# Kernel tuning notes

Hardware: AMD Instinct MI355X
Metric: run time of the kernel (lower is better)

Reference implementation:

```python
import jax, jax.numpy as jnp
import numpy as np

NEG_BIG = -9e15
ALPHA = 0.2  # LeakyReLU negative slope


def setup_inputs() -> dict:
    key = jax.random.key(0)
    k1, k2, k3, k4 = jax.random.split(key, 4)
    B, N, IN, OUT = 8, 2048, 128, 64
    x = jax.random.normal(k1, (B, N, IN), dtype=jnp.float32)
    adj = jax.random.randint(k2, (B, N, N), 0, 2, dtype=jnp.int32)
    # xavier_uniform with gain=1.414
    lim_W = 1.414 * np.sqrt(6.0 / (IN + OUT))
    W = jax.random.uniform(k3, (IN, OUT), jnp.float32, -lim_W, lim_W)
    lim_a = 1.414 * np.sqrt(6.0 / (2 * OUT + 1))
    a = jax.random.uniform(k4, (2 * OUT, 1), jnp.float32, -lim_a, lim_a)
    return {"x": x, "adj": adj, "W": W, "a": a}


def reference(x, adj, W, a):
    # h: [B, N, out_dim]
    h = jnp.matmul(x, W)
    out_dim = W.shape[1]
    a1 = a[:out_dim, 0]   # applied to h_i (row / destination)
    a2 = a[out_dim:, 0]   # applied to h_j (col / source)
    # e_ij = leakyrelu(h_i . a1 + h_j . a2)  -- avoids the O(B*N*N*2d) concat
    si = jnp.einsum('bnd,d->bn', h, a1)  # [B, N]
    sj = jnp.einsum('bnd,d->bn', h, a2)  # [B, N]
    e = si[:, :, None] + sj[:, None, :]  # [B, N, N]
    e = jnp.where(e > 0, e, ALPHA * e)   # LeakyReLU
    e = jnp.where(adj > 0, e, NEG_BIG)
    attention = jax.nn.softmax(e, axis=-1)  # [B, N, N]
    # dropout p=0.0 (eval mode): identity
    h_prime = jnp.matmul(attention, h)       # [B, N, out_dim]
    return h_prime, attention
```

## Files before the change

kernel.cpp:

```cpp
#include <hip/hip_runtime.h>

#define BB 8
#define NN 2048
#define IND 128
#define OUTD 64
#define ALPHA 0.2f

typedef __attribute__((ext_vector_type(8))) short bf16x8;
typedef __attribute__((ext_vector_type(4))) float f32x4;
typedef unsigned int u32;

__global__ __launch_bounds__(256) void k1_hproj(const float* __restrict__ x,
                                                const float* __restrict__ W,
                                                const float* __restrict__ a,
                                                short* __restrict__ hT_hi,
                                                short* __restrict__ hT_lo,
                                                float* __restrict__ si,
                                                float* __restrict__ sj) {
    __shared__ float Wl[IND * OUTD];
    __shared__ float xl[16][IND];
    __shared__ float tile[16][OUTD + 1];
    int t = threadIdx.x, lane = t & 63, wave = t >> 6;

    const float4* W4 = (const float4*)W;
    float4* Wl4 = (float4*)Wl;
    #pragma unroll
    for (int q = 0; q < 8; ++q) Wl4[t + q * 256] = W4[t + q * 256];

    int row0 = blockIdx.x * 16;
    const float4* x4 = (const float4*)(x + (size_t)row0 * IND);
    float4* xl4 = (float4*)&xl[0][0];
    xl4[t] = x4[t];
    xl4[t + 256] = x4[t + 256];
    __syncthreads();

    float a1v = a[lane];
    float a2v = a[OUTD + lane];

    float acc[4] = {0.f, 0.f, 0.f, 0.f};
    int rbase = wave * 4;
    for (int k = 0; k < IND; k += 4) {
        float4 xv0 = *(const float4*)&xl[rbase + 0][k];
        float4 xv1 = *(const float4*)&xl[rbase + 1][k];
        float4 xv2 = *(const float4*)&xl[rbase + 2][k];
        float4 xv3 = *(const float4*)&xl[rbase + 3][k];
        #pragma unroll
        for (int q = 0; q < 4; ++q) {
            float w = Wl[(k + q) * OUTD + lane];
            acc[0] = fmaf(((const float*)&xv0)[q], w, acc[0]);
            acc[1] = fmaf(((const float*)&xv1)[q], w, acc[1]);
            acc[2] = fmaf(((const float*)&xv2)[q], w, acc[2]);
            acc[3] = fmaf(((const float*)&xv3)[q], w, acc[3]);
        }
    }
    #pragma unroll
    for (int rr = 0; rr < 4; ++rr) {
        size_t grow = (size_t)row0 + rbase + rr;
        tile[rbase + rr][lane] = acc[rr];
        float v1 = acc[rr] * a1v;
        float v2 = acc[rr] * a2v;
        #pragma unroll
        for (int o = 32; o; o >>= 1) {
            v1 += __shfl_xor(v1, o);
            v2 += __shfl_xor(v2, o);
        }
        if (lane == 0) { si[grow] = v1; sj[grow] = v2; }
    }
    __syncthreads();

    int d = t >> 2, kq = (t & 3) * 4;
    int b = row0 >> 11;
    int krow = (row0 & (NN - 1)) + kq;
    float v0 = tile[kq + 0][d], v1 = tile[kq + 1][d];
    float v2 = tile[kq + 2][d], v3 = tile[kq + 3][d];
    u32 b0 = __float_as_uint(v0), b1 = __float_as_uint(v1);
    u32 b2 = __float_as_uint(v2), b3 = __float_as_uint(v3);
    u32 h0 = b0 & 0xffff0000u, h1 = b1 & 0xffff0000u;
    u32 h2 = b2 & 0xffff0000u, h3 = b3 & 0xffff0000u;
    float l0 = v0 - __uint_as_float(h0), l1 = v1 - __uint_as_float(h1);
    float l2 = v2 - __uint_as_float(h2), l3 = v3 - __uint_as_float(h3);
    uint2 hi2, lo2;
    hi2.x = (b0 >> 16) | h1;
    hi2.y = (b2 >> 16) | h3;
    lo2.x = (__float_as_uint(l0) >> 16) | (__float_as_uint(l1) & 0xffff0000u);
    lo2.y = (__float_as_uint(l2) >> 16) | (__float_as_uint(l3) & 0xffff0000u);
    size_t off = ((size_t)b * OUTD + d) * NN + krow;
    *(uint2*)(hT_hi + off) = hi2;
    *(uint2*)(hT_lo + off) = lo2;
}

__global__ __launch_bounds__(256) void k23(const int* __restrict__ adj,
                                           const float* __restrict__ si,
                                           const float* __restrict__ sj,
                                           const short* __restrict__ hT_hi,
                                           const short* __restrict__ hT_lo,
                                           float* __restrict__ attn,
                                           float* __restrict__ hp) {
    __shared__ unsigned char mask_lds[16][264];
    __shared__ float inv_lds[16];
    __shared__ f32x4 red[4][4][64];

    int t = threadIdx.x, lane = t & 63, w = t >> 6;
    int bk = blockIdx.x;
    int b = bk >> 7;
    int i0 = (bk & 127) * 16;
    size_t rowbase = (size_t)b * NN + i0;
    const float* sjb = sj + (size_t)b * NN;

    for (int rr = 0; rr < 4; ++rr) {
        int row = w * 4 + rr;
        size_t grow = rowbase + row;
        float s_i = si[grow];
        const int4* arow = (const int4*)(adj + grow * NN);
        float sum = 0.f;
        #pragma unroll
        for (int pass = 0; pass < 4; ++pass) {
            int jb = pass * 512 + lane * 8;
            int4 a0 = arow[pass * 128 + lane * 2];
            int4 a1 = arow[pass * 128 + lane * 2 + 1];
            float4 s0 = *(const float4*)(sjb + jb);
            float4 s1 = *(const float4*)(sjb + jb + 4);
            int av[8] = {a0.x, a0.y, a0.z, a0.w, a1.x, a1.y, a1.z, a1.w};
            float sv[8] = {s0.x, s0.y, s0.z, s0.w, s1.x, s1.y, s1.z, s1.w};
            unsigned mb = 0;
            #pragma unroll
            for (int q = 0; q < 8; ++q) {
                float e = s_i + sv[q];
                e = e > 0.f ? e : ALPHA * e;
                float pe = __expf(e);
                if (av[q] > 0) { mb |= 1u << q; sum += pe; }
            }
            mask_lds[row][pass * 64 + lane] = (unsigned char)mb;
        }
        #pragma unroll
        for (int o = 32; o; o >>= 1) sum += __shfl_xor(sum, o);
        if (lane == 0) inv_lds[row] = sum > 0.f ? 1.0f / sum : 0.f;
    }
    __syncthreads();

    int m = lane & 15, g = lane >> 4;
    float si_m = si[rowbase + m];
    float inv_m = inv_lds[m];
    float* arow_out = attn + (rowbase + m) * (size_t)NN;
    const short* bh_base = hT_hi + ((size_t)b * OUTD + m) * NN;
    const short* bl_base = hT_lo + ((size_t)b * OUTD + m) * NN;

    f32x4 acc[4];
    #pragma unroll
    for (int tt = 0; tt < 4; ++tt) acc[tt] = (f32x4){0.f, 0.f, 0.f, 0.f};

    for (int step = 0; step < 16; ++step) {
        int jb = w * 512 + step * 32 + g * 8;
        float4 s0 = *(const float4*)(sjb + jb);
        float4 s1 = *(const float4*)(sjb + jb + 4);
        unsigned mb = mask_lds[m][jb >> 3];
        float sv[8] = {s0.x, s0.y, s0.z, s0.w, s1.x, s1.y, s1.z, s1.w};
        float p[8];
        #pragma unroll
        for (int q = 0; q < 8; ++q) {
            float e = si_m + sv[q];
            e = e > 0.f ? e : ALPHA * e;
            float pe = __expf(e) * inv_m;
            p[q] = ((mb >> q) & 1) ? pe : 0.f;
        }
        *(float4*)(arow_out + jb) = make_float4(p[0], p[1], p[2], p[3]);
        *(float4*)(arow_out + jb + 4) = make_float4(p[4], p[5], p[6], p[7]);

        union { bf16x8 v; u32 u[4]; } ph, pl;
        #pragma unroll
        for (int q = 0; q < 4; ++q) {
            u32 c0 = __float_as_uint(p[2 * q]), c1 = __float_as_uint(p[2 * q + 1]);
            u32 t0 = c0 & 0xffff0000u, t1 = c1 & 0xffff0000u;
            float d0 = p[2 * q] - __uint_as_float(t0);
            float d1 = p[2 * q + 1] - __uint_as_float(t1);
            ph.u[q] = (c0 >> 16) | t1;
            pl.u[q] = (__float_as_uint(d0) >> 16) | (__float_as_uint(d1) & 0xffff0000u);
        }

        #pragma unroll
        for (int tt = 0; tt < 4; ++tt) {
            bf16x8 bh = *(const bf16x8*)(bh_base + (size_t)tt * 16 * NN + jb);
            bf16x8 bl = *(const bf16x8*)(bl_base + (size_t)tt * 16 * NN + jb);
            acc[tt] = __builtin_amdgcn_mfma_f32_16x16x32_bf16(ph.v, bh, acc[tt], 0, 0, 0);
            acc[tt] = __builtin_amdgcn_mfma_f32_16x16x32_bf16(ph.v, bl, acc[tt], 0, 0, 0);
            acc[tt] = __builtin_amdgcn_mfma_f32_16x16x32_bf16(pl.v, bh, acc[tt], 0, 0, 0);
        }
    }

    #pragma unroll
    for (int tt = 0; tt < 4; ++tt) red[w][tt][lane] = acc[tt];
    __syncthreads();

    for (int idx = t; idx < 16 * OUTD; idx += 256) {
        int row = idx >> 6, n = idx & 63;
        int ln = (row >> 2) * 16 + (n & 15);
        int reg = row & 3;
        float v = ((const float*)&red[0][n >> 4][ln])[reg]
                + ((const float*)&red[1][n >> 4][ln])[reg]
                + ((const float*)&red[2][n >> 4][ln])[reg]
                + ((const float*)&red[3][n >> 4][ln])[reg];
        hp[(rowbase + row) * OUTD + n] = v;
    }
}

extern "C" void kernel_launch(void* const* d_in, const int* in_sizes, int n_in,
                              void* d_out, int out_size, void* d_ws, size_t ws_size,
                              hipStream_t stream) {
    const float* x   = (const float*)d_in[0];
    const int*   adj = (const int*)d_in[1];
    const float* W   = (const float*)d_in[2];
    const float* a   = (const float*)d_in[3];

    float* out  = (float*)d_out;
    float* hp   = out;
    float* attn = out + (size_t)BB * NN * OUTD;

    char* ws = (char*)d_ws;
    short* hT_hi = (short*)ws;
    short* hT_lo = hT_hi + (size_t)BB * OUTD * NN;
    float* si    = (float*)(hT_lo + (size_t)BB * OUTD * NN);
    float* sj    = si + (size_t)BB * NN;

    k1_hproj<<<BB * NN / 16, 256, 0, stream>>>(x, W, a, hT_hi, hT_lo, si, sj);
    k23<<<BB * NN / 16, 256, 0, stream>>>(adj, si, sj, hT_hi, hT_lo, attn, hp);
}
```

Measured before the change: 130.6 us.

## Split adjacency mask pass into separate kernel and coalesce attention writes

Moves the adjacency scan and softmax denominator computation into its own kernel, which writes a packed bit mask and inverse sums to workspace, using one wave per row across many more blocks. The attention-plus-PV kernel then reads the mask from global memory and writes the attention matrix in a fully coalesced row-major loop rather than the strided per-lane layout tied to the MFMA fragment. The aim is to raise parallelism on the adj-reading phase and improve store coalescing for the large attention output. The cost is an extra launch, an extra global mask round-trip, and exp being computed twice for the PV stage.

```diff
diff --git a/kernel.cpp b/kernel.cpp
--- a/kernel.cpp
+++ b/kernel.cpp
@@ -89,15 +89,51 @@
     *(uint2*)(hT_lo + off) = lo2;
 }
 
-__global__ __launch_bounds__(256) void k23(const int* __restrict__ adj,
-                                           const float* __restrict__ si,
-                                           const float* __restrict__ sj,
-                                           const short* __restrict__ hT_hi,
-                                           const short* __restrict__ hT_lo,
-                                           float* __restrict__ attn,
-                                           float* __restrict__ hp) {
-    __shared__ unsigned char mask_lds[16][264];
-    __shared__ float inv_lds[16];
+__global__ __launch_bounds__(256) void k2_mask(const int* __restrict__ adj,
+                                               const float* __restrict__ si,
+                                               const float* __restrict__ sj,
+                                               float* __restrict__ invS,
+                                               unsigned char* __restrict__ mask) {
+    int t = threadIdx.x, lane = t & 63, w = t >> 6;
+    int row = blockIdx.x * 4 + w;
+    int b = row >> 11;
+    float s_i = si[row];
+    const int4* arow = (const int4*)(adj + (size_t)row * NN);
+    const float* sjb = sj + (size_t)b * NN;
+
+    float sum = 0.f;
+    #pragma unroll
+    for (int q = 0; q < 8; ++q) {
+        int4 av = arow[q * 64 + lane];
+        float4 sv = *(const float4*)(sjb + q * 256 + lane * 4);
+        unsigned nib = 0;
+        float e, pe;
+        e = s_i + sv.x; e = e > 0.f ? e : ALPHA * e; pe = __expf(e);
+        if (av.x > 0) { nib |= 1u; sum += pe; }
+        e = s_i + sv.y; e = e > 0.f ? e : ALPHA * e; pe = __expf(e);
+        if (av.y > 0) { nib |= 2u; sum += pe; }
+        e = s_i + sv.z; e = e > 0.f ? e : ALPHA * e; pe = __expf(e);
+        if (av.z > 0) { nib |= 4u; sum += pe; }
+        e = s_i + sv.w; e = e > 0.f ? e : ALPHA * e; pe = __expf(e);
+        if (av.w > 0) { nib |= 8u; sum += pe; }
+        unsigned pn = (unsigned)__shfl_xor((int)nib, 1);
+        if (!(lane & 1))
+            mask[(size_t)row * 256 + q * 32 + (lane >> 1)] = (unsigned char)(nib | (pn << 4));
+    }
+    #pragma unroll
+    for (int o = 32; o; o >>= 1) sum += __shfl_xor(sum, o);
+    if (lane == 0) invS[row] = sum > 0.f ? 1.0f / sum : 0.f;
+}
+
+__global__ __launch_bounds__(256) void k3_attn_pv(const unsigned char* __restrict__ mask,
+                                                  const float* __restrict__ si,
+                                                  const float* __restrict__ sj,
+                                                  const float* __restrict__ invS,
+                                                  const short* __restrict__ hT_hi,
+                                                  const short* __restrict__ hT_lo,
+                                                  float* __restrict__ attn,
+                                                  float* __restrict__ hp) {
+    __shared__ float si_s[16], inv_s[16];
     __shared__ f32x4 red[4][4][64];
 
     int t = threadIdx.x, lane = t & 63, w = t >> 6;
@@ -107,41 +143,37 @@
     size_t rowbase = (size_t)b * NN + i0;
     const float* sjb = sj + (size_t)b * NN;
 
-    for (int rr = 0; rr < 4; ++rr) {
-        int row = w * 4 + rr;
-        size_t grow = rowbase + row;
-        float s_i = si[grow];
-        const int4* arow = (const int4*)(adj + grow * NN);
-        float sum = 0.f;
-        #pragma unroll
-        for (int pass = 0; pass < 4; ++pass) {
-            int jb = pass * 512 + lane * 8;
-            int4 a0 = arow[pass * 128 + lane * 2];
-            int4 a1 = arow[pass * 128 + lane * 2 + 1];
-            float4 s0 = *(const float4*)(sjb + jb);
-            float4 s1 = *(const float4*)(sjb + jb + 4);
-            int av[8] = {a0.x, a0.y, a0.z, a0.w, a1.x, a1.y, a1.z, a1.w};
-            float sv[8] = {s0.x, s0.y, s0.z, s0.w, s1.x, s1.y, s1.z, s1.w};
-            unsigned mb = 0;
-            #pragma unroll
-            for (int q = 0; q < 8; ++q) {
-                float e = s_i + sv[q];
-                e = e > 0.f ? e : ALPHA * e;
-                float pe = __expf(e);
-                if (av[q] > 0) { mb |= 1u << q; sum += pe; }
-            }
-            mask_lds[row][pass * 64 + lane] = (unsigned char)mb;
-        }
-        #pragma unroll
-        for (int o = 32; o; o >>= 1) sum += __shfl_xor(sum, o);
-        if (lane == 0) inv_lds[row] = sum > 0.f ? 1.0f / sum : 0.f;
-    }
-    __syncthreads();
+    if (t < 16) {
+        si_s[t] = si[rowbase + t];
+        inv_s[t] = invS[rowbase + t];
+    }
+    __syncthreads();
+
+    #pragma unroll 4
+    for (int it = 0; it < 32; ++it) {
+        int idx = it * 256 + t;
+        int row = idx >> 9;
+        int col = (idx & 511) << 2;
+        float4 sv = *(const float4*)(sjb + col);
+        unsigned char mb = mask[(rowbase + row) * 256 + (col >> 3)];
+        unsigned nib = (mb >> (col & 4)) & 0xFu;
+        float s_i = si_s[row], inv = inv_s[row];
+        float4 pv;
+        float e;
+        e = s_i + sv.x; e = e > 0.f ? e : ALPHA * e;
+        pv.x = (nib & 1u) ? __expf(e) * inv : 0.f;
+        e = s_i + sv.y; e = e > 0.f ? e : ALPHA * e;
+        pv.y = (nib & 2u) ? __expf(e) * inv : 0.f;
+        e = s_i + sv.z; e = e > 0.f ? e : ALPHA * e;
+        pv.z = (nib & 4u) ? __expf(e) * inv : 0.f;
+        e = s_i + sv.w; e = e > 0.f ? e : ALPHA * e;
+        pv.w = (nib & 8u) ? __expf(e) * inv : 0.f;
+        *(float4*)(attn + (rowbase + row) * (size_t)NN + col) = pv;
+    }
 
     int m = lane & 15, g = lane >> 4;
-    float si_m = si[rowbase + m];
-    float inv_m = inv_lds[m];
-    float* arow_out = attn + (rowbase + m) * (size_t)NN;
+    float si_m = si_s[m];
+    float inv_m = inv_s[m];
     const short* bh_base = hT_hi + ((size_t)b * OUTD + m) * NN;
     const short* bl_base = hT_lo + ((size_t)b * OUTD + m) * NN;
 
@@ -153,7 +185,7 @@
         int jb = w * 512 + step * 32 + g * 8;
         float4 s0 = *(const float4*)(sjb + jb);
         float4 s1 = *(const float4*)(sjb + jb + 4);
-        unsigned mb = mask_lds[m][jb >> 3];
+        unsigned mb = mask[(rowbase + m) * 256 + (jb >> 3)];
         float sv[8] = {s0.x, s0.y, s0.z, s0.w, s1.x, s1.y, s1.z, s1.w};
         float p[8];
         #pragma unroll
@@ -161,10 +193,8 @@
             float e = si_m + sv[q];
             e = e > 0.f ? e : ALPHA * e;
             float pe = __expf(e) * inv_m;
-            p[q] = ((mb >> q) & 1) ? pe : 0.f;
-        }
-        *(float4*)(arow_out + jb) = make_float4(p[0], p[1], p[2], p[3]);
-        *(float4*)(arow_out + jb + 4) = make_float4(p[4], p[5], p[6], p[7]);
+            p[q] = ((mb >> q) & 1u) ? pe : 0.f;
+        }
 
         union { bf16x8 v; u32 u[4]; } ph, pl;
         #pragma unroll
@@ -220,7 +250,10 @@
     short* hT_lo = hT_hi + (size_t)BB * OUTD * NN;
     float* si    = (float*)(hT_lo + (size_t)BB * OUTD * NN);
     float* sj    = si + (size_t)BB * NN;
+    float* invS  = sj + (size_t)BB * NN;
+    unsigned char* mask = (unsigned char*)(invS + (size_t)BB * NN);
 
     k1_hproj<<<BB * NN / 16, 256, 0, stream>>>(x, W, a, hT_hi, hT_lo, si, sj);
-    k23<<<BB * NN / 16, 256, 0, stream>>>(adj, si, sj, hT_hi, hT_lo, attn, hp);
-}
+    k2_mask<<<BB * NN / 4, 256, 0, stream>>>(adj, si, sj, invS, mask);
+    k3_attn_pv<<<BB * NN / 16, 256, 0, stream>>>(mask, si, sj, invS, hT_hi, hT_lo, attn, hp);
+}
```

Measured after the change: 156.1 us. 19.5% more time.
